# Kernel tuning notes

Measured on AMD Instinct MI355X. Metric: run time of the kernel, lower is better.

## Reference

```python
import jax, jax.numpy as jnp
import numpy as np

B, C, L = 4, 512, 4096
LN_EPS = 1e-5


def setup_inputs() -> dict:
    key = jax.random.key(0)
    ks = jax.random.split(key, 6)
    s = 1.0 / np.sqrt(C)
    return {
        "x": jax.random.normal(ks[0], (B, C, L), dtype=jnp.float32),
        "ln_w": jnp.ones((C,), dtype=jnp.float32),
        "ln_b": jnp.zeros((C,), dtype=jnp.float32),
        "wq": jax.random.normal(ks[1], (C, C), dtype=jnp.float32) * s,
        "bq": jnp.zeros((C,), dtype=jnp.float32),
        "wk": jax.random.normal(ks[2], (C, C), dtype=jnp.float32) * s,
        "bk": jnp.zeros((C,), dtype=jnp.float32),
        "wv": jax.random.normal(ks[3], (C, C), dtype=jnp.float32) * s,
        "bv": jnp.zeros((C,), dtype=jnp.float32),
        "wp": jax.random.normal(ks[4], (C, C), dtype=jnp.float32) * s,
        "bp": jnp.zeros((C,), dtype=jnp.float32),
    }


def reference(x, ln_w, ln_b, wq, bq, wk, bk, wv, bv, wp, bp):
    # x: [b, c, l]. LayerNorm over channels (permute -> LN -> permute back).
    xt = jnp.swapaxes(x, 1, 2)  # [b, l, c]
    mu = jnp.mean(xt, axis=-1, keepdims=True)
    var = jnp.var(xt, axis=-1, keepdims=True)
    h = (xt - mu) * jax.lax.rsqrt(var + LN_EPS) * ln_w + ln_b  # [b, l, c]

    # 1x1 convs == channel-mixing matmuls (weight [out, in])
    q = jnp.einsum('blc,oc->blo', h, wq) + bq  # [b, l, c]
    k = jnp.einsum('blc,oc->blo', h, wk) + bk
    v = jnp.einsum('blc,oc->blo', h, wv) + bv

    c = x.shape[1]
    scores = jnp.einsum('blc,bmc->blm', q, k) * (float(c) ** -0.5)  # [b, l_q, l_k]
    attn = jax.nn.softmax(scores, axis=-1)
    o = jnp.einsum('blm,bmc->blc', attn, v)  # [b, l, c]

    o = jnp.einsum('blc,oc->blo', o, wp) + bp
    o = jax.nn.selu(o)
    return x + jnp.swapaxes(o, 1, 2)  # [b, c, l]
```

## Files before the change

### kernel.cpp

```cpp
#include <hip/hip_runtime.h>


typedef __attribute__((ext_vector_type(8))) __bf16 bf16x8;
typedef __attribute__((ext_vector_type(4))) __bf16 bf16x4;
typedef __attribute__((ext_vector_type(4))) float  f32x4;

__device__ __forceinline__ f32x4 mfma16(bf16x8 a, bf16x8 b, f32x4 c) {
  return __builtin_amdgcn_mfma_f32_16x16x32_bf16(a, b, c, 0, 0, 0);
}

__device__ __forceinline__ void gll16(const void* g, void* l) {
  __builtin_amdgcn_global_load_lds(
      (const __attribute__((address_space(1))) unsigned int*)g,
      (__attribute__((address_space(3))) unsigned int*)l, 16, 0, 0);
}

__device__ __forceinline__ float selu_f(float v) {
  return 1.0507009873554805f * (v > 0.f ? v : 1.6732632423543772f * (__expf(v) - 1.f));
}

#define QSCALE ((float)(1.4426950408889634 / 22.627416997969522))

__global__ __launch_bounds__(256) void cvt_w(const float* __restrict__ w0,
                                             const float* __restrict__ w1,
                                             const float* __restrict__ w2,
                                             const float* __restrict__ w3,
                                             __bf16* __restrict__ dst) {
  int idx = blockIdx.x * 256 + threadIdx.x;
  int which = idx >> 16;
  const float* s = which == 0 ? w0 : which == 1 ? w1 : which == 2 ? w2 : w3;
  f32x4 v = *(const f32x4*)(s + (size_t)(idx & 65535) * 4);
  bf16x4 o = {(__bf16)v.x, (__bf16)v.y, (__bf16)v.z, (__bf16)v.w};
  *(bf16x4*)(dst + (size_t)idx * 4) = o;
}

__global__ __launch_bounds__(256) void ln_stats(const float* __restrict__ x,
                                                float* __restrict__ mu,
                                                float* __restrict__ rs) {
  __shared__ float shs[4][64], shq[4][64];
  int b = blockIdx.y, l0 = blockIdx.x * 64;
  int i = threadIdx.x & 63, j = threadIdx.x >> 6;
  const float* xp = x + (size_t)b * 512 * 4096 + l0 + i;
  float s = 0.f, sq = 0.f;
  for (int c = j; c < 512; c += 4) {
    float v = xp[(size_t)c * 4096];
    s += v; sq += v * v;
  }
  shs[j][i] = s; shq[j][i] = sq;
  __syncthreads();
  if (threadIdx.x < 64) {
    float S = shs[0][i] + shs[1][i] + shs[2][i] + shs[3][i];
    float Q = shq[0][i] + shq[1][i] + shq[2][i] + shq[3][i];
    float m = S * (1.f / 512.f);
    float var = Q * (1.f / 512.f) - m * m;
    int idx = b * 4096 + l0 + i;
    mu[idx] = m;
    rs[idx] = rsqrtf(var + 1e-5f);
  }
}

__global__ __launch_bounds__(256) void ln_apply(const float* __restrict__ x,
                                                const float* __restrict__ mu,
                                                const float* __restrict__ rs,
                                                const float* __restrict__ lw,
                                                const float* __restrict__ lb,
                                                __bf16* __restrict__ h) {
  __shared__ float t[64][65];
  int b = blockIdx.z, c0 = blockIdx.y * 64, l0 = blockIdx.x * 64;
  int li = threadIdx.x & 63, r4 = threadIdx.x >> 6;
  const float* xp = x + (size_t)(b * 512 + c0) * 4096 + l0;
#pragma unroll
  for (int rr = 0; rr < 16; ++rr) {
    int cl = rr * 4 + r4;
    t[cl][li] = xp[(size_t)cl * 4096 + li];
  }
  __syncthreads();
  float gw = lw[c0 + li], gb = lb[c0 + li];
#pragma unroll
  for (int rr = 0; rr < 16; ++rr) {
    int lr = rr * 4 + r4;
    int l = l0 + lr;
    float m = mu[b * 4096 + l], r = rs[b * 4096 + l];
    float v = (t[li][lr] - m) * r * gw + gb;
    h[((size_t)b * 4096 + l) * 512 + c0 + li] = (__bf16)v;
  }
}

__global__ __launch_bounds__(256, 2) void gemm_qkv(
    const __bf16* __restrict__ A, const __bf16* __restrict__ W,
    const float* __restrict__ b0, const float* __restrict__ b1,
    const float* __restrict__ b2, __bf16* __restrict__ out,
    __bf16* __restrict__ vt) {
  __shared__ __align__(16) __bf16 As[128 * 128];
  __shared__ __align__(16) __bf16 Bs[128 * 128];
  const int tid = threadIdx.x;
  const int w = tid >> 6, lane = tid & 63, g = lane >> 4, li = lane & 15;
  const int id = blockIdx.x;
  const int jj = id >> 3;
  const int m0 = (16 * (id & 7) + jj / 12) * 128;
  const int n0 = (jj % 12) * 128;
  const int wm = w >> 1, wn = w & 1;
  const int srow = lane >> 4;
  f32x4 acc[4][4] = {};
  for (int kt = 0; kt < 4; ++kt) {
    __syncthreads();
#pragma unroll
    for (int qq = 0; qq < 8; ++qq) {
      int r = w * 32 + qq * 4;
      int gr = (lane & 15) ^ (4 * (qq & 1) + srow);
      gll16(A + (size_t)(m0 + r + srow) * 512 + kt * 128 + gr * 8, &As[r * 128]);
      gll16(W + (size_t)(n0 + r + srow) * 512 + kt * 128 + gr * 8, &Bs[r * 128]);
    }
    __syncthreads();
#pragma unroll
    for (int kk = 0; kk < 4; ++kk) {
      bf16x8 af[4], bf[4];
#pragma unroll
      for (int t = 0; t < 4; ++t) {
        int ra = wm * 64 + t * 16 + li;
        af[t] = *(const bf16x8*)&As[ra * 128 + ((kk * 32 + 8 * g) ^ ((ra & 7) * 8))];
        int rb = wn * 64 + t * 16 + li;
        bf[t] = *(const bf16x8*)&Bs[rb * 128 + ((kk * 32 + 8 * g) ^ ((rb & 7) * 8))];
      }
#pragma unroll
      for (int i = 0; i < 4; ++i)
#pragma unroll
        for (int j = 0; j < 4; ++j) acc[i][j] = mfma16(af[i], bf[j], acc[i][j]);
    }
  }
  const int which = n0 >> 9;
  if (which < 2) {
    const float* bb = which == 0 ? b0 : b1;
    const float sc = which == 0 ? QSCALE : 1.0f;
    __bf16* o = out + (size_t)which * 8388608;
#pragma unroll
    for (int i = 0; i < 4; ++i) {
#pragma unroll
      for (int j = 0; j < 4; ++j) {
        int r = m0 + wm * 64 + i * 16 + 4 * g;
        int c = (n0 & 511) + wn * 64 + j * 16 + li;
        float bv = bb[c];
#pragma unroll
        for (int e = 0; e < 4; ++e)
          o[(size_t)(r + e) * 512 + c] = (__bf16)((acc[i][j][e] + bv) * sc);
      }
    }
  } else {
#pragma unroll
    for (int i = 0; i < 4; ++i) {
#pragma unroll
      for (int j = 0; j < 4; ++j) {
        int r = m0 + wm * 64 + i * 16 + 4 * g;
        int c = (n0 & 511) + wn * 64 + j * 16 + li;
        float bv = b2[c];
#pragma unroll
        for (int e = 0; e < 4; ++e) {
          int row = r + e;
          vt[((size_t)(row >> 12) * 512 + c) * 4096 + (row & 4095)] =
              (__bf16)(acc[i][j][e] + bv);
        }
      }
    }
  }
}

__global__ __launch_bounds__(256, 2) void gemm_pp(
    const __bf16* __restrict__ A, const __bf16* __restrict__ Bm,
    const float* __restrict__ bias, const float* __restrict__ xres,
    float* __restrict__ out) {
  __shared__ __align__(16) __bf16 As[128 * 128];
  __shared__ __align__(16) __bf16 Bs[128 * 128];
  const int tid = threadIdx.x;
  const int w = tid >> 6, lane = tid & 63, g = lane >> 4, li = lane & 15;
  const int id = blockIdx.x;
  const int jj = id >> 3;
  const int n0 = (16 * (id & 7) + (jj & 15)) * 128;
  const int m0 = (jj >> 4) * 128;
  const int wm = w >> 1, wn = w & 1;
  const int srow = lane >> 4;
  f32x4 acc[4][4] = {};
  for (int kt = 0; kt < 4; ++kt) {
    __syncthreads();
#pragma unroll
    for (int qq = 0; qq < 8; ++qq) {
      int r = w * 32 + qq * 4;
      int gr = (lane & 15) ^ (4 * (qq & 1) + srow);
      gll16(A + (size_t)(m0 + r + srow) * 512 + kt * 128 + gr * 8, &As[r * 128]);
      gll16(Bm + (size_t)(n0 + r + srow) * 512 + kt * 128 + gr * 8, &Bs[r * 128]);
    }
    __syncthreads();
#pragma unroll
    for (int kk = 0; kk < 4; ++kk) {
      bf16x8 af[4], bf[4];
#pragma unroll
      for (int t = 0; t < 4; ++t) {
        int ra = wm * 64 + t * 16 + li;
        af[t] = *(const bf16x8*)&As[ra * 128 + ((kk * 32 + 8 * g) ^ ((ra & 7) * 8))];
        int rb = wn * 64 + t * 16 + li;
        bf[t] = *(const bf16x8*)&Bs[rb * 128 + ((kk * 32 + 8 * g) ^ ((rb & 7) * 8))];
      }
#pragma unroll
      for (int i = 0; i < 4; ++i)
#pragma unroll
        for (int j = 0; j < 4; ++j) acc[i][j] = mfma16(af[i], bf[j], acc[i][j]);
    }
  }
#pragma unroll
  for (int i = 0; i < 4; ++i) {
#pragma unroll
    for (int j = 0; j < 4; ++j) {
      int r = m0 + wm * 64 + i * 16 + 4 * g;
      int c = n0 + wn * 64 + j * 16 + li;
      int bb = c >> 12, l = c & 4095;
#pragma unroll
      for (int e = 0; e < 4; ++e) {
        float v = acc[i][j][e] + bias[r + e];
        size_t oi = ((size_t)bb * 512 + (r + e)) * 4096 + l;
        out[oi] = xres[oi] + selu_f(v);
      }
    }
  }
}

__global__ __launch_bounds__(512, 2) void flash_half(
    const __bf16* __restrict__ Q, const __bf16* __restrict__ K,
    const __bf16* __restrict__ VT, __bf16* __restrict__ Op,
    float* __restrict__ stats) {
  __shared__ __align__(16) __bf16 Ks[64][512];
  __shared__ __align__(16) __bf16 VTs[512][64];
  __shared__ __align__(16) __bf16 Ps[128][64];

  const int tid = threadIdx.x;
  const int w = tid >> 6, lane = tid & 63, g = lane >> 4, li = lane & 15;
  const int id = blockIdx.x;
  const int grp = id & 7;
  const int b = grp >> 1, half = grp & 1;
  const int q0 = (id >> 3) * 128;
  const size_t base = (size_t)b * (4096 * 512);
  const int kvbase = half * 2048;

  bf16x8 qf[16];
  {
    const __bf16* qp = Q + base + (size_t)(q0 + 16 * w + li) * 512 + 8 * g;
#pragma unroll
    for (int ks = 0; ks < 16; ++ks) qf[ks] = *(const bf16x8*)(qp + ks * 32);
  }

  f32x4 acc[8][4] = {};
  f32x4 lacc = {};
  bf16x8 ones;
#pragma unroll
  for (int j = 0; j < 8; ++j) ones[j] = (__bf16)1.0f;

  auto stageK = [&](int kt) {
#pragma unroll
    for (int i = 0; i < 8; ++i) {
      int r = w * 8 + i;
      int y = (lane * 16) ^ ((r & 7) << 4);
      gll16(K + base + (size_t)(kvbase + kt * 64 + r) * 512 + (y >> 1),
            &Ks[r][0]);
    }
  };
  auto stageVT = [&](int kt) {
    const int drow = lane >> 3;
    const int gr = (lane & 7) ^ drow;
#pragma unroll
    for (int i = 0; i < 8; ++i) {
      int d0 = w * 64 + i * 8;
      gll16(VT + (size_t)b * 2097152 + (size_t)(d0 + drow) * 4096 +
                kvbase + kt * 64 + gr * 8,
            &VTs[d0][0]);
    }
  };

  stageK(0);
  stageVT(0);
  __syncthreads();

  for (int kt = 0; kt < 32; ++kt) {
    __builtin_amdgcn_s_setprio(1);
    f32x4 s[4] = {};
#pragma unroll
    for (int ks = 0; ks < 16; ++ks) {
      int e = (ks * 32 + 8 * g) ^ ((li & 7) * 8);
#pragma unroll
      for (int kvt = 0; kvt < 4; ++kvt) {
        bf16x8 kf = *(const bf16x8*)&Ks[kvt * 16 + li][e];
        s[kvt] = mfma16(qf[ks], kf, s[kvt]);
      }
    }
    __builtin_amdgcn_s_setprio(0);

#pragma unroll
    for (int kvt = 0; kvt < 4; ++kvt) {
#pragma unroll
      for (int e = 0; e < 4; ++e) {
        float p = exp2f(s[kvt][e]);
        int row = 16 * w + 4 * g + e;
        int slot = (2 * kvt + (li >> 3)) ^ (row & 7);
        Ps[row][slot * 8 + (li & 7)] = (__bf16)p;
      }
    }
    __syncthreads();

    if (kt + 1 < 32) stageK(kt + 1);

#pragma unroll
    for (int ks = 0; ks < 2; ++ks) {
      bf16x8 bfr[4];
#pragma unroll
      for (int ct = 0; ct < 4; ++ct) {
        int dcol = 64 * w + 16 * ct + li;
        int slot = (4 * ks + g) ^ (li & 7);
        bfr[ct] = *(const bf16x8*)&VTs[dcol][slot * 8];
      }
      __builtin_amdgcn_s_setprio(1);
#pragma unroll
      for (int rt = 0; rt < 8; ++rt) {
        int prow = rt * 16 + li;
        int slot = (4 * ks + g) ^ (li & 7);
        bf16x8 af = *(const bf16x8*)&Ps[prow][slot * 8];
        if (rt == w) lacc = mfma16(af, ones, lacc);
#pragma unroll
        for (int ct = 0; ct < 4; ++ct)
          acc[rt][ct] = mfma16(af, bfr[ct], acc[rt][ct]);
      }
      __builtin_amdgcn_s_setprio(0);
    }
    __syncthreads();

    if (kt + 1 < 32) stageVT(kt + 1);
  }

  if (li == 0)
    *(f32x4*)(stats + half * 16384 + b * 4096 + q0 + 16 * w + 4 * g) = lacc;
#pragma unroll
  for (int rt = 0; rt < 8; ++rt) {
#pragma unroll
    for (int ct = 0; ct < 4; ++ct) {
      int rr = q0 + rt * 16 + 4 * g;
      int cc = w * 64 + ct * 16 + li;
#pragma unroll
      for (int e = 0; e < 4; ++e)
        Op[(size_t)half * 8388608 + base + (size_t)(rr + e) * 512 + cc] =
            (__bf16)acc[rt][ct][e];
    }
  }
}

__global__ __launch_bounds__(256) void combine2(const __bf16* __restrict__ Op,
                                                const float* __restrict__ stats,
                                                __bf16* __restrict__ ao) {
  int gid = blockIdx.x * 256 + threadIdx.x;
  int row = gid >> 6;
  int c = (gid & 63) * 8;
  float l0 = stats[row], l1 = stats[16384 + row];
  float inv = 1.f / (l0 + l1);
  bf16x8 v0 = *(const bf16x8*)(Op + (size_t)row * 512 + c);
  bf16x8 v1 = *(const bf16x8*)(Op + 8388608 + (size_t)row * 512 + c);
  bf16x8 o;
#pragma unroll
  for (int j = 0; j < 8; ++j)
    o[j] = (__bf16)(((float)v0[j] + (float)v1[j]) * inv);
  *(bf16x8*)(ao + (size_t)row * 512 + c) = o;
}

extern "C" void kernel_launch(void* const* d_in, const int* in_sizes, int n_in,
                              void* d_out, int out_size, void* d_ws, size_t ws_size,
                              hipStream_t stream) {
  const float* x   = (const float*)d_in[0];
  const float* lnw = (const float*)d_in[1];
  const float* lnb = (const float*)d_in[2];
  const float* wq  = (const float*)d_in[3];
  const float* bq  = (const float*)d_in[4];
  const float* wk  = (const float*)d_in[5];
  const float* bk  = (const float*)d_in[6];
  const float* wv  = (const float*)d_in[7];
  const float* bv  = (const float*)d_in[8];
  const float* wp  = (const float*)d_in[9];
  const float* bp  = (const float*)d_in[10];

  char* ws = (char*)d_ws;
  const size_t MB = 1024 * 1024;
  __bf16* h    = (__bf16*)(ws);
  __bf16* q    = (__bf16*)(ws + 16 * MB);
  __bf16* vt   = (__bf16*)(ws + 48 * MB);
  __bf16* wbf  = (__bf16*)(ws + 64 * MB);
  float*  mu   = (float*)(ws + 66 * MB);
  float*  rsg  = (float*)(ws + 66 * MB + 65536);
  __bf16* op   = (__bf16*)(ws + 67 * MB);
  float*  stats= (float*)(ws + 99 * MB);
  __bf16* ao   = h;

  cvt_w<<<1024, 256, 0, stream>>>(wq, wk, wv, wp, wbf);
  ln_stats<<<dim3(64, 4), 256, 0, stream>>>(x, mu, rsg);
  ln_apply<<<dim3(64, 8, 4), 256, 0, stream>>>(x, mu, rsg, lnw, lnb, h);
  gemm_qkv<<<1536, 256, 0, stream>>>(h, wbf, bq, bk, bv, q, vt);
  flash_half<<<256, 512, 0, stream>>>(q, q + 8388608, vt, op, stats);
  combine2<<<4096, 256, 0, stream>>>(op, stats, ao);
  gemm_pp<<<512, 256, 0, stream>>>(wbf + 3 * 262144, ao, bp, x,
                                   (float*)d_out);
}
```

Measured before the change: 319.2 us.

## Fuse LayerNorm kernels and stage GEMM/flash epilogues through LDS for coalesced stores

Merges ln_stats and ln_apply into one kernel that computes per-position stats with vectorized loads and then normalizes and transposes in the same block, so the mu/rs round trip and one launch go away. The QKV GEMM epilogue now writes tiles into shared memory and emits 16-byte coalesced stores, including a transposed V layout through a padded LDS tile instead of scattered 2-byte writes. The flash kernel's output store is staged the same way. The fused LN launches only 256 blocks, which lowers parallelism, and the staged epilogues add extra barriers.

```diff
diff --git a/kernel.cpp b/kernel.cpp
--- a/kernel.cpp
+++ b/kernel.cpp
@@ -34,55 +34,65 @@
   *(bf16x4*)(dst + (size_t)idx * 4) = o;
 }
 
-__global__ __launch_bounds__(256) void ln_stats(const float* __restrict__ x,
-                                                float* __restrict__ mu,
-                                                float* __restrict__ rs) {
-  __shared__ float shs[4][64], shq[4][64];
-  int b = blockIdx.y, l0 = blockIdx.x * 64;
-  int i = threadIdx.x & 63, j = threadIdx.x >> 6;
-  const float* xp = x + (size_t)b * 512 * 4096 + l0 + i;
-  float s = 0.f, sq = 0.f;
-  for (int c = j; c < 512; c += 4) {
-    float v = xp[(size_t)c * 4096];
-    s += v; sq += v * v;
-  }
-  shs[j][i] = s; shq[j][i] = sq;
-  __syncthreads();
-  if (threadIdx.x < 64) {
-    float S = shs[0][i] + shs[1][i] + shs[2][i] + shs[3][i];
-    float Q = shq[0][i] + shq[1][i] + shq[2][i] + shq[3][i];
-    float m = S * (1.f / 512.f);
-    float var = Q * (1.f / 512.f) - m * m;
-    int idx = b * 4096 + l0 + i;
-    mu[idx] = m;
-    rs[idx] = rsqrtf(var + 1e-5f);
-  }
-}
-
-__global__ __launch_bounds__(256) void ln_apply(const float* __restrict__ x,
-                                                const float* __restrict__ mu,
-                                                const float* __restrict__ rs,
+__global__ __launch_bounds__(256) void ln_fused(const float* __restrict__ x,
                                                 const float* __restrict__ lw,
                                                 const float* __restrict__ lb,
                                                 __bf16* __restrict__ h) {
-  __shared__ float t[64][65];
-  int b = blockIdx.z, c0 = blockIdx.y * 64, l0 = blockIdx.x * 64;
-  int li = threadIdx.x & 63, r4 = threadIdx.x >> 6;
-  const float* xp = x + (size_t)(b * 512 + c0) * 4096 + l0;
-#pragma unroll
-  for (int rr = 0; rr < 16; ++rr) {
-    int cl = rr * 4 + r4;
-    t[cl][li] = xp[(size_t)cl * 4096 + li];
+  __shared__ float red[16][16][4][2];
+  __shared__ float smu[64], srs[64];
+  __shared__ float t2[64][65];
+  const int b = blockIdx.y, l0 = blockIdx.x * 64;
+  const int tid = threadIdx.x;
+  const int hi = tid >> 4, lq = tid & 15;
+
+  {
+    const float* xp = x + (size_t)b * 2097152 + l0 + lq * 4;
+    float s[4] = {0.f, 0.f, 0.f, 0.f}, qq[4] = {0.f, 0.f, 0.f, 0.f};
+    for (int it = 0; it < 32; ++it) {
+      int c = it * 16 + hi;
+      f32x4 v = *(const f32x4*)(xp + (size_t)c * 4096);
+#pragma unroll
+      for (int k = 0; k < 4; ++k) { s[k] += v[k]; qq[k] += v[k] * v[k]; }
+    }
+#pragma unroll
+    for (int k = 0; k < 4; ++k) {
+      red[hi][lq][k][0] = s[k];
+      red[hi][lq][k][1] = qq[k];
+    }
   }
   __syncthreads();
-  float gw = lw[c0 + li], gb = lb[c0 + li];
-#pragma unroll
-  for (int rr = 0; rr < 16; ++rr) {
-    int lr = rr * 4 + r4;
-    int l = l0 + lr;
-    float m = mu[b * 4096 + l], r = rs[b * 4096 + l];
-    float v = (t[li][lr] - m) * r * gw + gb;
-    h[((size_t)b * 4096 + l) * 512 + c0 + li] = (__bf16)v;
+  if (tid < 64) {
+    int lqq = tid >> 2, k = tid & 3;
+    float S = 0.f, Q = 0.f;
+    for (int hh = 0; hh < 16; ++hh) {
+      S += red[hh][lqq][k][0];
+      Q += red[hh][lqq][k][1];
+    }
+    float m = S * (1.f / 512.f);
+    float var = Q * (1.f / 512.f) - m * m;
+    smu[lqq * 4 + k] = m;
+    srs[lqq * 4 + k] = rsqrtf(var + 1e-5f);
+  }
+  __syncthreads();
+
+  const int li = tid & 63, r4 = tid >> 6;
+  for (int cb = 0; cb < 8; ++cb) {
+    int c0 = cb * 64;
+    const float* xq = x + (size_t)(b * 512 + c0) * 4096 + l0;
+#pragma unroll
+    for (int rr = 0; rr < 16; ++rr) {
+      int cl = rr * 4 + r4;
+      t2[cl][li] = xq[(size_t)cl * 4096 + li];
+    }
+    __syncthreads();
+    float gw = lw[c0 + li], gb = lb[c0 + li];
+#pragma unroll
+    for (int rr = 0; rr < 16; ++rr) {
+      int lr = rr * 4 + r4;
+      float v = (t2[li][lr] - smu[lr]) * srs[lr] * gw + gb;
+      h[((size_t)b * 4096 + l0 + lr) * 512 + c0 + li] = (__bf16)v;
+    }
+    __syncthreads();
   }
 }
 
@@ -91,8 +101,9 @@
     const float* __restrict__ b0, const float* __restrict__ b1,
     const float* __restrict__ b2, __bf16* __restrict__ out,
     __bf16* __restrict__ vt) {
-  __shared__ __align__(16) __bf16 As[128 * 128];
-  __shared__ __align__(16) __bf16 Bs[128 * 128];
+  __shared__ __align__(16) __bf16 smem[2 * 128 * 128];
+  __bf16* As = smem;
+  __bf16* Bs = smem + 16384;
   const int tid = threadIdx.x;
   const int w = tid >> 6, lane = tid & 63, g = lane >> 4, li = lane & 15;
   const int id = blockIdx.x;
@@ -129,37 +140,52 @@
     }
   }
   const int which = n0 >> 9;
+  __syncthreads();
   if (which < 2) {
     const float* bb = which == 0 ? b0 : b1;
     const float sc = which == 0 ? QSCALE : 1.0f;
+#pragma unroll
+    for (int i = 0; i < 4; ++i) {
+#pragma unroll
+      for (int j = 0; j < 4; ++j) {
+        int rl = wm * 64 + i * 16 + 4 * g;
+        int cl = wn * 64 + j * 16 + li;
+        float bv = bb[(n0 & 511) + cl];
+#pragma unroll
+        for (int e = 0; e < 4; ++e)
+          smem[(rl + e) * 128 + cl] = (__bf16)((acc[i][j][e] + bv) * sc);
+      }
+    }
+    __syncthreads();
     __bf16* o = out + (size_t)which * 8388608;
 #pragma unroll
+    for (int rep = 0; rep < 8; ++rep) {
+      int ii = rep * 256 + tid;
+      int row = ii >> 4, col8 = (ii & 15) * 8;
+      *(bf16x8*)&o[(size_t)(m0 + row) * 512 + (n0 & 511) + col8] =
+          *(const bf16x8*)&smem[row * 128 + col8];
+    }
+  } else {
+#pragma unroll
     for (int i = 0; i < 4; ++i) {
 #pragma unroll
       for (int j = 0; j < 4; ++j) {
-        int r = m0 + wm * 64 + i * 16 + 4 * g;
-        int c = (n0 & 511) + wn * 64 + j * 16 + li;
-        float bv = bb[c];
-#pragma unroll
-        for (int e = 0; e < 4; ++e)
-          o[(size_t)(r + e) * 512 + c] = (__bf16)((acc[i][j][e] + bv) * sc);
-      }
-    }
-  } else {
-#pragma unroll
-    for (int i = 0; i < 4; ++i) {
-#pragma unroll
-      for (int j = 0; j < 4; ++j) {
-        int r = m0 + wm * 64 + i * 16 + 4 * g;
-        int c = (n0 & 511) + wn * 64 + j * 16 + li;
-        float bv = b2[c];
-#pragma unroll
-        for (int e = 0; e < 4; ++e) {
-          int row = r + e;
-          vt[((size_t)(row >> 12) * 512 + c) * 4096 + (row & 4095)] =
-              (__bf16)(acc[i][j][e] + bv);
-        }
-      }
+        int rl = wm * 64 + i * 16 + 4 * g;
+        int cl = wn * 64 + j * 16 + li;
+        float bv = b2[(n0 & 511) + cl];
+        bf16x4 pk = {(__bf16)(acc[i][j][0] + bv), (__bf16)(acc[i][j][1] + bv),
+                     (__bf16)(acc[i][j][2] + bv), (__bf16)(acc[i][j][3] + bv)};
+        *(bf16x4*)&smem[cl * 136 + rl] = pk;
+      }
+    }
+    __syncthreads();
+    const int bb_ = m0 >> 12, l0_ = m0 & 4095;
+#pragma unroll
+    for (int rep = 0; rep < 8; ++rep) {
+      int chan = rep * 16 + (tid >> 4);
+      int l8 = (tid & 15) * 8;
+      *(bf16x8*)&vt[((size_t)(bb_ * 512) + (n0 & 511) + chan) * 4096 + l0_ + l8] =
+          *(const bf16x8*)&smem[chan * 136 + l8];
     }
   }
 }
@@ -334,16 +360,23 @@
 
   if (li == 0)
     *(f32x4*)(stats + half * 16384 + b * 4096 + q0 + 16 * w + 4 * g) = lacc;
-#pragma unroll
+
+  __bf16* C = &Ps[0][0];
   for (int rt = 0; rt < 8; ++rt) {
-#pragma unroll
-    for (int ct = 0; ct < 4; ++ct) {
-      int rr = q0 + rt * 16 + 4 * g;
-      int cc = w * 64 + ct * 16 + li;
+    __syncthreads();
+#pragma unroll
+    for (int ct = 0; ct < 4; ++ct)
 #pragma unroll
       for (int e = 0; e < 4; ++e)
-        Op[(size_t)half * 8388608 + base + (size_t)(rr + e) * 512 + cc] =
-            (__bf16)acc[rt][ct][e];
+        C[(4 * g + e) * 512 + 64 * w + 16 * ct + li] = (__bf16)acc[rt][ct][e];
+    __syncthreads();
+#pragma unroll
+    for (int rep = 0; rep < 2; ++rep) {
+      int ii = rep * 512 + tid;
+      int row16 = ii >> 6, col8 = (ii & 63) * 8;
+      *(bf16x8*)&Op[(size_t)half * 8388608 + base +
+                    (size_t)(q0 + rt * 16 + row16) * 512 + col8] =
+          *(const bf16x8*)&C[row16 * 512 + col8];
     }
   }
 }
@@ -386,15 +419,12 @@
   __bf16* q    = (__bf16*)(ws + 16 * MB);
   __bf16* vt   = (__bf16*)(ws + 48 * MB);
   __bf16* wbf  = (__bf16*)(ws + 64 * MB);
-  float*  mu   = (float*)(ws + 66 * MB);
-  float*  rsg  = (float*)(ws + 66 * MB + 65536);
   __bf16* op   = (__bf16*)(ws + 67 * MB);
   float*  stats= (float*)(ws + 99 * MB);
   __bf16* ao   = h;
 
   cvt_w<<<1024, 256, 0, stream>>>(wq, wk, wv, wp, wbf);
-  ln_stats<<<dim3(64, 4), 256, 0, stream>>>(x, mu, rsg);
-  ln_apply<<<dim3(64, 8, 4), 256, 0, stream>>>(x, mu, rsg, lnw, lnb, h);
+  ln_fused<<<dim3(64, 4), 256, 0, stream>>>(x, lnw, lnb, h);
   gemm_qkv<<<1536, 256, 0, stream>>>(h, wbf, bq, bk, bv, q, vt);
   flash_half<<<256, 512, 0, stream>>>(q, q + 8388608, vt, op, stats);
   combine2<<<4096, 256, 0, stream>>>(op, stats, ao);
```

Result: faster. 288.8 us (-9.5%).
